# Kernel optimization log

Hardware: AMD Instinct MI355X
Metric: run time of the kernel (lower is better)

## Reference

```python
import jax, jax.numpy as jnp
import numpy as np

SEQ_LEN = 8192
D_MODEL = 1024
D_K = 128
D_V = 128


def setup_inputs() -> dict:
    key = jax.random.key(0)
    kx, kq, kk, kv = jax.random.split(key, 4)
    # xavier-uniform scale for (out, in) linear weights
    def xavier(k, out_f, in_f):
        lim = np.sqrt(6.0 / (in_f + out_f))
        return jax.random.uniform(k, (out_f, in_f), jnp.float32, -lim, lim)
    return {
        "X": jax.random.normal(kx, (SEQ_LEN, D_MODEL), jnp.float32),
        "Wq": xavier(kq, D_K, D_MODEL),
        "Wk": xavier(kk, D_K, D_MODEL),
        "Wv": xavier(kv, D_V, D_MODEL),
    }


def reference(X, Wq, Wk, Wv):
    # X: (S, d_model); W*: (d_k, d_model) torch Linear weights (y = x @ W.T)
    S = X.shape[0]
    Q = X @ Wq.T                      # (S, d_k)
    K = X @ Wk.T                      # (S, d_k)
    V = X @ Wv.T                      # (S, d_v)
    scale = jnp.sqrt(jnp.asarray(D_K, X.dtype))
    scores = (Q @ K.T) / scale        # (S, S)
    causal = jnp.tril(jnp.ones((S, S), bool))
    scores = jnp.where(causal, scores, -jnp.inf)
    weights = jax.nn.softmax(scores, axis=1)
    # dropout p=0.0 -> identity
    Z = weights @ V                   # (S, d_v)
    return Z
```

## Files before the change

### kernel.cpp

```cpp
#include <hip/hip_runtime.h>
#include <hip/hip_bf16.h>

#define S_LEN 8192
#define DM    1024
#define DK    128
#define KSTR  136
#define VSTR  72
#define SLOTD 1056

typedef __attribute__((ext_vector_type(8))) short bf16x8;
typedef __attribute__((ext_vector_type(8))) _Float16 f16x8;
typedef __attribute__((ext_vector_type(4))) float f32x4;

__device__ __forceinline__ f32x4 mfma16(bf16x8 a, bf16x8 b, f32x4 c) {
    return __builtin_amdgcn_mfma_f32_16x16x32_bf16(a, b, c, 0, 0, 0);
}

__device__ __forceinline__ ushort f2bf(float f) {
    unsigned u = __builtin_bit_cast(unsigned, f);
    u += 0x7FFFu + ((u >> 16) & 1u);
    return (ushort)(u >> 16);
}

__device__ __forceinline__ ushort f2h(float f) {
    return __builtin_bit_cast(ushort, (_Float16)f);
}

__device__ __forceinline__ uint cvt_pk_bf16(float a, float b) {
    uint r;
    asm("v_cvt_pk_bf16_f32 %0, %1, %2" : "=v"(r) : "v"(a), "v"(b));
    return r;
}

__global__ __launch_bounds__(256, 1)
void convert_kernel(const float* __restrict__ X,
                    const float* __restrict__ Wq,
                    const float* __restrict__ Wk,
                    const float* __restrict__ Wv,
                    _Float16* __restrict__ Xh,
                    _Float16* __restrict__ Wh) {
    const int NX4 = S_LEN * DM / 4;
    const int NW4 = DK * DM / 4;
    const int total4 = NX4 + 3 * NW4;
    for (int i = blockIdx.x * 256 + threadIdx.x; i < total4; i += gridDim.x * 256) {
        const float4* src;
        _Float16* dst;
        int off;
        if (i < NX4) {
            src = (const float4*)X; dst = Xh; off = i;
        } else {
            const int w = i - NX4;
            const int which = w / NW4;
            off = w - which * NW4;
            src = (const float4*)(which == 0 ? Wq : (which == 1 ? Wk : Wv));
            dst = Wh + which * (DK * DM);
        }
        const float4 v = src[off];
        union { _Float16 h[4]; uint2 u; } p;
        p.h[0] = (_Float16)v.x; p.h[1] = (_Float16)v.y;
        p.h[2] = (_Float16)v.z; p.h[3] = (_Float16)v.w;
        *(uint2*)(dst + (size_t)off * 4) = p.u;
    }
}

__global__ __launch_bounds__(256)
void proj_gemm_kernel(const _Float16* __restrict__ Xh,
                      const _Float16* __restrict__ Wh,
                      ushort* __restrict__ Qb,
                      ushort* __restrict__ Kb,
                      ushort* __restrict__ Vtb) {
    __shared__ _Float16 Ash[32 * 32];
    __shared__ _Float16 Bsh[128 * 32];

    const int tid  = threadIdx.x;
    const int lane = tid & 63;
    const int quad = lane >> 4;
    const int l15  = lane & 15;
    const int wv   = tid >> 6;
    const int wm   = wv & 1;
    const int wn   = wv >> 1;
    const int m0   = blockIdx.x * 32;
    const int nb   = blockIdx.y;
    const _Float16* Wbase = Wh + nb * (DK * DM);

    f32x4 acc[4];
#pragma unroll
    for (int ni = 0; ni < 4; ++ni) acc[ni] = (f32x4){0.f, 0.f, 0.f, 0.f};

    for (int kk = 0; kk < DM; kk += 32) {
        __syncthreads();
        for (int s = tid; s < 640; s += 256) {
            if (s < 128) {
                const int row = s >> 2, sg = s & 3;
                __builtin_amdgcn_global_load_lds(
                    (const __attribute__((address_space(1))) void*)(Xh + (size_t)(m0 + row) * DM + kk + sg * 8),
                    (__attribute__((address_space(3))) void*)(Ash + s * 8), 16, 0, 0);
            } else {
                const int t = s - 128;
                const int row = t >> 2, sg = t & 3;
                __builtin_amdgcn_global_load_lds(
                    (const __attribute__((address_space(1))) void*)(Wbase + (size_t)row * DM + kk + sg * 8),
                    (__attribute__((address_space(3))) void*)(Bsh + t * 8), 16, 0, 0);
            }
        }
        __syncthreads();

        const f16x8 af = *(const f16x8*)(Ash + (wm * 16 + l15) * 32 + quad * 8);
        f16x8 bf[4];
#pragma unroll
        for (int t = 0; t < 4; ++t)
            bf[t] = *(const f16x8*)(Bsh + (wn * 64 + t * 16 + l15) * 32 + quad * 8);
#pragma unroll
        for (int ni = 0; ni < 4; ++ni)
            acc[ni] = __builtin_amdgcn_mfma_f32_16x16x32_f16(af, bf[ni], acc[ni], 0, 0, 0);
    }

    if (nb == 2) {
#pragma unroll
        for (int ni = 0; ni < 4; ++ni) {
            const int n = wn * 64 + ni * 16 + l15;
            const int m = m0 + wm * 16 + quad * 4;
            union { ushort h[4]; uint2 u; } p;
#pragma unroll
            for (int r = 0; r < 4; ++r) p.h[r] = f2bf(acc[ni][r]);
            *(uint2*)(Vtb + (size_t)n * S_LEN + m) = p.u;
        }
    } else {
        ushort* Ob = (nb == 0) ? Qb : Kb;
        const float sc = (nb == 0) ? 0.088388347648318447f * 1.4426950408889634f : 1.0f;
#pragma unroll
        for (int ni = 0; ni < 4; ++ni) {
            const int n = wn * 64 + ni * 16 + l15;
#pragma unroll
            for (int r = 0; r < 4; ++r) {
                const int m = m0 + wm * 16 + quad * 4 + r;
                Ob[(size_t)m * DK + n] = f2bf(acc[ni][r] * sc);
            }
        }
    }
}

__global__ __launch_bounds__(256, 3)
void flash_partial_kernel(const ushort* __restrict__ Qg,
                          const ushort* __restrict__ Kg,
                          const ushort* __restrict__ Vtg,
                          float* __restrict__ Part) {
    __shared__ __align__(16) ushort Ks [64 * KSTR];
    __shared__ __align__(16) ushort Vts[128 * VSTR];

    const int b = 995 - (int)blockIdx.x;
    int qb, chunk;
    if (b < 36) {
        int q = 0;
        while (b >= (q + 1) * (q + 2) / 2) ++q;
        qb = q; chunk = b - q * (q + 1) / 2;
    } else {
        qb = 8 + ((b - 36) >> 3);
        chunk = (b - 36) & 7;
    }
    const int nkt   = qb + 1;
    const int NC    = nkt < 8 ? nkt : 8;
    const int kt_lo = chunk * nkt / NC;
    const int kt_hi = (chunk + 1) * nkt / NC;

    const int tid  = threadIdx.x;
    const int wv   = tid >> 6;
    const int lane = tid & 63;
    const int quad = lane >> 4;
    const int l15  = lane & 15;
    const int q0w  = qb * 64 + wv * 16;

    bf16x8 qf[4];
    {
        const ushort* qrow = Qg + (size_t)(q0w + l15) * DK + quad * 8;
#pragma unroll
        for (int kc = 0; kc < 4; ++kc) qf[kc] = *(const bf16x8*)(qrow + kc * 32);
    }

    float m_ = -__builtin_inff();
    float l_ = 0.f;
    f32x4 acc[8];
#pragma unroll
    for (int d = 0; d < 8; ++d) acc[d] = (f32x4){0.f, 0.f, 0.f, 0.f};

    bf16x8 stg[8];
#define LOAD_TILE(K0)                                                          \
    {                                                                          \
        const int k0_ = (K0);                                                  \
        _Pragma("unroll")                                                      \
        for (int i = 0; i < 8; ++i) {                                          \
            const int c = tid + (i << 8);                                      \
            if (c < 1024) {                                                    \
                const int row = c >> 4, ch = c & 15;                           \
                stg[i] = *(const bf16x8*)(Kg + (size_t)(k0_ + row) * DK + ch * 8); \
            } else {                                                           \
                const int cc = c - 1024;                                       \
                const int row = cc >> 3, ch = cc & 7;                          \
                stg[i] = *(const bf16x8*)(Vtg + (size_t)row * S_LEN + k0_ + ch * 8); \
            }                                                                  \
        }                                                                      \
    }

    LOAD_TILE(kt_lo * 64)

    for (int kt = kt_lo; kt < kt_hi; ++kt) {
        const int k0 = kt * 64;

        __syncthreads();
#pragma unroll
        for (int i = 0; i < 8; ++i) {
            const int c = tid + (i << 8);
            if (c < 1024) {
                const int row = c >> 4, ch = c & 15;
                *(bf16x8*)(Ks + row * KSTR + ch * 8) = stg[i];
            } else {
                const int cc = c - 1024;
                const int row = cc >> 3, ch = cc & 7;
                const int s_lo = ((ch >> 2) << 5) + ((ch & 1) << 4) + (((ch >> 1) & 1) << 2);
                union { bf16x8 v; uint2 q2[2]; } u;
                u.v = stg[i];
                ushort* vb = Vts + row * VSTR + s_lo;
                *(uint2*)vb       = u.q2[0];
                *(uint2*)(vb + 8) = u.q2[1];
            }
        }
        if (kt + 1 < kt_hi) LOAD_TILE((kt + 1) * 64)
        __syncthreads();

        f32x4 Sr[4];
        __builtin_amdgcn_s_setprio(1);
#pragma unroll
        for (int nb = 0; nb < 4; ++nb) {
            Sr[nb] = (f32x4){0.f, 0.f, 0.f, 0.f};
            const ushort* kb = Ks + (nb * 16 + l15) * KSTR + quad * 8;
#pragma unroll
            for (int kc = 0; kc < 4; ++kc)
                Sr[nb] = mfma16(*(const bf16x8*)(kb + kc * 32), qf[kc], Sr[nb]);
        }
        __builtin_amdgcn_s_setprio(0);

        if (k0 + 63 > q0w) {
            const int qg = q0w + l15;
#pragma unroll
            for (int nb = 0; nb < 4; ++nb) {
                const int kg = k0 + nb * 16 + quad * 4;
#pragma unroll
                for (int r = 0; r < 4; ++r)
                    if (kg + r > qg) Sr[nb][r] = -__builtin_inff();
            }
        }

        float pmax;
        {
            float a0 = fmaxf(fmaxf(Sr[0][0], Sr[0][1]), fmaxf(Sr[0][2], Sr[0][3]));
            float a1 = fmaxf(fmaxf(Sr[1][0], Sr[1][1]), fmaxf(Sr[1][2], Sr[1][3]));
            float a2 = fmaxf(fmaxf(Sr[2][0], Sr[2][1]), fmaxf(Sr[2][2], Sr[2][3]));
            float a3 = fmaxf(fmaxf(Sr[3][0], Sr[3][1]), fmaxf(Sr[3][2], Sr[3][3]));
            pmax = fmaxf(fmaxf(a0, a1), fmaxf(a2, a3));
            pmax = fmaxf(pmax, __shfl_xor(pmax, 16));
            pmax = fmaxf(pmax, __shfl_xor(pmax, 32));
        }
        if (__any(pmax > m_ + 8.f)) {
            const float mnew = fmaxf(m_, pmax);
            const float al = __builtin_amdgcn_exp2f(m_ - mnew);
            m_ = mnew;
            l_ *= al;
            float alr[4];
#pragma unroll
            for (int r = 0; r < 4; ++r)
                alr[r] = __shfl(al, (lane & 48) | (((lane >> 4) & 3) * 4 + r));
#pragma unroll
            for (int d = 0; d < 8; ++d)
#pragma unroll
                for (int r = 0; r < 4; ++r) acc[d][r] *= alr[r];
        }

        float p[4][4];
        float rs = 0.f;
#pragma unroll
        for (int nb = 0; nb < 4; ++nb)
#pragma unroll
            for (int r = 0; r < 4; ++r) {
                p[nb][r] = __builtin_amdgcn_exp2f(Sr[nb][r] - m_);
                rs += p[nb][r];
            }
        rs += __shfl_xor(rs, 16);
        rs += __shfl_xor(rs, 32);
        l_ += rs;

        __builtin_amdgcn_s_setprio(1);
#pragma unroll
        for (int kcp = 0; kcp < 2; ++kcp) {
            union { uint u[4]; bf16x8 v; } pf;
            pf.u[0] = cvt_pk_bf16(p[2 * kcp][0],     p[2 * kcp][1]);
            pf.u[1] = cvt_pk_bf16(p[2 * kcp][2],     p[2 * kcp][3]);
            pf.u[2] = cvt_pk_bf16(p[2 * kcp + 1][0], p[2 * kcp + 1][1]);
            pf.u[3] = cvt_pk_bf16(p[2 * kcp + 1][2], p[2 * kcp + 1][3]);
#pragma unroll
            for (int db = 0; db < 8; ++db) {
                const bf16x8 vf = *(const bf16x8*)(Vts + (db * 16 + l15) * VSTR + kcp * 32 + quad * 8);
                acc[db] = mfma16(pf.v, vf, acc[db]);
            }
        }
        __builtin_amdgcn_s_setprio(0);
    }
#undef LOAD_TILE

    const int qt16 = qb * 4 + wv;
    float* slot = Part + (size_t)(qt16 * 8 + chunk) * SLOTD;
    if (quad == 0) {
        slot[l15]      = m_;
        slot[16 + l15] = l_;
    }
    uint* slotO = (uint*)(slot + 32);
#pragma unroll
    for (int d = 0; d < 8; ++d)
#pragma unroll
        for (int r = 0; r < 4; ++r) {
            const float v  = acc[d][r];
            const float vp = __shfl_xor(v, 1);
            if ((l15 & 1) == 0) {
                const int row = quad * 4 + r;
                const uint u = (uint)f2h(v) | ((uint)f2h(vp) << 16);
                slotO[(row * 128 + d * 16 + l15) >> 1] = u;
            }
        }
}

__global__ __launch_bounds__(256)
void flash_merge_kernel(const float* __restrict__ Part, float* __restrict__ Out) {
    __shared__ float Ms[16], Ls[16];
    __shared__ float Sc[8][16];
    const int qt = blockIdx.x;
    const int q0 = qt * 16;
    const int qb = qt >> 2;
    const int P  = (qb + 1 < 8) ? (qb + 1) : 8;
    const int tid = threadIdx.x;
    const float* base = Part + (size_t)qt * 8 * SLOTD;

    if (tid < 16) {
        float M = -__builtin_inff();
        for (int p = 0; p < P; ++p) M = fmaxf(M, base[p * SLOTD + tid]);
        float L = 0.f;
        for (int p = 0; p < P; ++p)
            L += base[p * SLOTD + 16 + tid] * exp2f(base[p * SLOTD + tid] - M);
        Ms[tid] = M; Ls[tid] = L;
    }
    __syncthreads();
    if (tid < 128) {
        const int p = tid >> 4, row = tid & 15;
        Sc[p][row] = (p < P) ? exp2f(base[p * SLOTD + row] - Ms[row]) : 0.f;
    }
    __syncthreads();

#pragma unroll
    for (int j = tid; j < 1024; j += 256) {
        const int row = j >> 6, c2 = j & 63;
        float o0 = 0.f, o1 = 0.f;
        for (int p = 0; p < P; ++p) {
            const uint u = ((const uint*)(base + p * SLOTD + 32))[row * 64 + c2];
            const float sc = Sc[p][row];
            o0 += (float)__builtin_bit_cast(_Float16, (ushort)(u & 0xFFFF)) * sc;
            o1 += (float)__builtin_bit_cast(_Float16, (ushort)(u >> 16)) * sc;
        }
        const float inv = 1.0f / Ls[row];
        float2 o; o.x = o0 * inv; o.y = o1 * inv;
        *(float2*)(Out + (size_t)(q0 + row) * DK + c2 * 2) = o;
    }
}

extern "C" void kernel_launch(void* const* d_in, const int* in_sizes, int n_in,
                              void* d_out, int out_size, void* d_ws, size_t ws_size,
                              hipStream_t stream) {
    const float* X  = (const float*)d_in[0];
    const float* Wq = (const float*)d_in[1];
    const float* Wk = (const float*)d_in[2];
    const float* Wv = (const float*)d_in[3];
    ushort* ws  = (ushort*)d_ws;
    ushort* Qb  = ws;
    ushort* Kb  = ws + (size_t)S_LEN * DK;
    ushort* Vtb = ws + 2 * (size_t)S_LEN * DK;
    _Float16* Xh = (_Float16*)(ws + 3 * (size_t)S_LEN * DK);
    _Float16* Wh = Xh + (size_t)S_LEN * DM;
    float* Part = (float*)Xh;
    float* Out = (float*)d_out;

    convert_kernel<<<1024, 256, 0, stream>>>(X, Wq, Wk, Wv, Xh, Wh);
    proj_gemm_kernel<<<dim3(256, 3), 256, 0, stream>>>(Xh, Wh, Qb, Kb, Vtb);
    flash_partial_kernel<<<996, 256, 0, stream>>>(Qb, Kb, Vtb, Part);
    flash_merge_kernel<<<512, 256, 0, stream>>>(Part, Out);
}
```

Measured before the change: 158.3 us.

## Switch flash attention to 32x32 MFMA with 128-row query blocks and double-buffered LDS

Restructures the partial attention kernel so each wave handles 32 query rows using 32x32x16 bf16 MFMA instead of 16x16x32, and each block covers 128 queries. K/V tiles are double-buffered in LDS so there is one barrier per tile instead of two, and waves skip fully masked tiles. The split-K chunking is redone (up to 16 chunks per query block, 544 blocks), and the merge kernel is widened to match. This aims to raise MFMA efficiency and K/V reuse and to cut synchronization, at the cost of more registers, lower occupancy (2 blocks per CU) and larger partial buffers.

Measured after the change: 171.0 us. 8.0% more time.

```diff
diff --git a/kernel.cpp b/kernel.cpp
--- a/kernel.cpp
+++ b/kernel.cpp
@@ -6,14 +6,19 @@
 #define DK    128
 #define KSTR  136
 #define VSTR  72
-#define SLOTD 1056
+#define SLOTD 2112
+#define NCMAX 16
 
 typedef __attribute__((ext_vector_type(8))) short bf16x8;
 typedef __attribute__((ext_vector_type(8))) _Float16 f16x8;
 typedef __attribute__((ext_vector_type(4))) float f32x4;
+typedef __attribute__((ext_vector_type(16))) float f32x16;
 
 __device__ __forceinline__ f32x4 mfma16(bf16x8 a, bf16x8 b, f32x4 c) {
     return __builtin_amdgcn_mfma_f32_16x16x32_bf16(a, b, c, 0, 0, 0);
+}
+__device__ __forceinline__ f32x16 mfma32(bf16x8 a, bf16x8 b, f32x16 c) {
+    return __builtin_amdgcn_mfma_f32_32x32x16_bf16(a, b, c, 0, 0, 0);
 }
 
 __device__ __forceinline__ ushort f2bf(float f) {
@@ -140,48 +145,49 @@
     }
 }
 
-__global__ __launch_bounds__(256, 3)
+__global__ __launch_bounds__(256, 2)
 void flash_partial_kernel(const ushort* __restrict__ Qg,
                           const ushort* __restrict__ Kg,
                           const ushort* __restrict__ Vtg,
                           float* __restrict__ Part) {
-    __shared__ __align__(16) ushort Ks [64 * KSTR];
-    __shared__ __align__(16) ushort Vts[128 * VSTR];
-
-    const int b = 995 - (int)blockIdx.x;
-    int qb, chunk;
-    if (b < 36) {
-        int q = 0;
-        while (b >= (q + 1) * (q + 2) / 2) ++q;
-        qb = q; chunk = b - q * (q + 1) / 2;
-    } else {
-        qb = 8 + ((b - 36) >> 3);
-        chunk = (b - 36) & 7;
-    }
-    const int nkt   = qb + 1;
-    const int NC    = nkt < 8 ? nkt : 8;
+    __shared__ __align__(16) ushort Ks [2][64 * KSTR];
+    __shared__ __align__(16) ushort Vts[2][128 * VSTR];
+
+    int rem = 543 - (int)blockIdx.x;
+    int qb = 0;
+    for (;;) {
+        const int nc = (2 * qb + 9) >> 3;
+        if (rem < nc) break;
+        rem -= nc; ++qb;
+    }
+    const int NC    = (2 * qb + 9) >> 3;
+    const int chunk = rem;
+    const int nkt   = 2 * qb + 2;
     const int kt_lo = chunk * nkt / NC;
     const int kt_hi = (chunk + 1) * nkt / NC;
 
     const int tid  = threadIdx.x;
     const int wv   = tid >> 6;
     const int lane = tid & 63;
-    const int quad = lane >> 4;
-    const int l15  = lane & 15;
-    const int q0w  = qb * 64 + wv * 16;
-
-    bf16x8 qf[4];
+    const int l31  = lane & 31;
+    const int hi   = lane >> 5;
+    const int q0w  = qb * 128 + wv * 32;
+    const int qrow = q0w + l31;
+
+    bf16x8 qf[8];
     {
-        const ushort* qrow = Qg + (size_t)(q0w + l15) * DK + quad * 8;
-#pragma unroll
-        for (int kc = 0; kc < 4; ++kc) qf[kc] = *(const bf16x8*)(qrow + kc * 32);
+        const ushort* qp = Qg + (size_t)qrow * DK + hi * 8;
+#pragma unroll
+        for (int i = 0; i < 8; ++i) qf[i] = *(const bf16x8*)(qp + i * 16);
     }
 
     float m_ = -__builtin_inff();
     float l_ = 0.f;
-    f32x4 acc[8];
-#pragma unroll
-    for (int d = 0; d < 8; ++d) acc[d] = (f32x4){0.f, 0.f, 0.f, 0.f};
+    f32x16 acc[4];
+#pragma unroll
+    for (int dt = 0; dt < 4; ++dt)
+#pragma unroll
+        for (int j = 0; j < 16; ++j) acc[dt][j] = 0.f;
 
     bf16x8 stg[8];
 #define LOAD_TILE(K0)                                                          \
@@ -200,165 +206,174 @@
             }                                                                  \
         }                                                                      \
     }
+#define WRITE_BUF(B)                                                           \
+    {                                                                          \
+        ushort* Kb_ = Ks[B]; ushort* Vb_ = Vts[B];                             \
+        _Pragma("unroll")                                                      \
+        for (int i = 0; i < 8; ++i) {                                          \
+            const int c = tid + (i << 8);                                      \
+            if (c < 1024) {                                                    \
+                const int row = c >> 4, ch = c & 15;                           \
+                *(bf16x8*)(Kb_ + row * KSTR + ch * 8) = stg[i];                \
+            } else {                                                           \
+                const int cc = c - 1024;                                       \
+                const int row = cc >> 3, ch = cc & 7;                          \
+                const int s_lo = ((ch & 1) << 2) + (((ch >> 1) & 1) << 4) + ((ch >> 2) << 5); \
+                union { bf16x8 v; uint2 q2[2]; } u;                            \
+                u.v = stg[i];                                                  \
+                ushort* vb = Vb_ + row * VSTR + s_lo;                          \
+                *(uint2*)vb       = u.q2[0];                                   \
+                *(uint2*)(vb + 8) = u.q2[1];                                   \
+            }                                                                  \
+        }                                                                      \
+    }
 
     LOAD_TILE(kt_lo * 64)
+    WRITE_BUF(0)
+    if (kt_lo + 1 < kt_hi) LOAD_TILE((kt_lo + 1) * 64)
+    __syncthreads();
 
     for (int kt = kt_lo; kt < kt_hi; ++kt) {
         const int k0 = kt * 64;
-
+        const int cb = (kt - kt_lo) & 1;
+        const ushort* ks = Ks[cb];
+        const ushort* vs = Vts[cb];
+        const bool prc = (k0 <= q0w);
+
+        f32x16 Sr0, Sr1;
+        if (prc) {
+            __builtin_amdgcn_s_setprio(1);
+#pragma unroll
+            for (int j = 0; j < 16; ++j) { Sr0[j] = 0.f; Sr1[j] = 0.f; }
+            const ushort* ka0 = ks + l31 * KSTR + hi * 8;
+            const ushort* ka1 = ka0 + 32 * KSTR;
+#pragma unroll
+            for (int i = 0; i < 8; ++i)
+                Sr0 = mfma32(*(const bf16x8*)(ka0 + i * 16), qf[i], Sr0);
+#pragma unroll
+            for (int i = 0; i < 8; ++i)
+                Sr1 = mfma32(*(const bf16x8*)(ka1 + i * 16), qf[i], Sr1);
+            __builtin_amdgcn_s_setprio(0);
+        }
+
+        if (kt + 1 < kt_hi) {
+            WRITE_BUF(cb ^ 1)
+            if (kt + 2 < kt_hi) LOAD_TILE((kt + 2) * 64)
+        }
+
+        if (prc) {
+            if (k0 + 63 > q0w) {
+#pragma unroll
+                for (int r = 0; r < 16; ++r) {
+                    const int krow = (r & 3) + 8 * (r >> 2) + 4 * hi;
+                    if (k0 + krow > qrow)      Sr0[r] = -__builtin_inff();
+                    if (k0 + 32 + krow > qrow) Sr1[r] = -__builtin_inff();
+                }
+            }
+
+            float pmax = Sr0[0];
+#pragma unroll
+            for (int r = 1; r < 16; ++r) pmax = fmaxf(pmax, Sr0[r]);
+#pragma unroll
+            for (int r = 0; r < 16; ++r) pmax = fmaxf(pmax, Sr1[r]);
+            pmax = fmaxf(pmax, __shfl_xor(pmax, 32));
+            if (__any(pmax > m_ + 8.f)) {
+                const float mnew = fmaxf(m_, pmax);
+                const float al = __builtin_amdgcn_exp2f(m_ - mnew);
+                m_ = mnew;
+                l_ *= al;
+#pragma unroll
+                for (int dt = 0; dt < 4; ++dt)
+#pragma unroll
+                    for (int j = 0; j < 16; ++j) acc[dt][j] *= al;
+            }
+            float rs = 0.f;
+            uint pfa[16];
+            {
+                float p0[16], p1[16];
+#pragma unroll
+                for (int r = 0; r < 16; ++r) { p0[r] = __builtin_amdgcn_exp2f(Sr0[r] - m_); rs += p0[r]; }
+#pragma unroll
+                for (int r = 0; r < 16; ++r) { p1[r] = __builtin_amdgcn_exp2f(Sr1[r] - m_); rs += p1[r]; }
+#pragma unroll
+                for (int j = 0; j < 4; ++j) {
+                    pfa[j]      = cvt_pk_bf16(p0[2 * j],     p0[2 * j + 1]);
+                    pfa[4 + j]  = cvt_pk_bf16(p0[8 + 2 * j], p0[8 + 2 * j + 1]);
+                    pfa[8 + j]  = cvt_pk_bf16(p1[2 * j],     p1[2 * j + 1]);
+                    pfa[12 + j] = cvt_pk_bf16(p1[8 + 2 * j], p1[8 + 2 * j + 1]);
+                }
+            }
+            rs += __shfl_xor(rs, 32);
+            l_ += rs;
+
+            __builtin_amdgcn_s_setprio(1);
+#pragma unroll
+            for (int kc = 0; kc < 4; ++kc) {
+                union { uint u[4]; bf16x8 v; } pu;
+#pragma unroll
+                for (int j = 0; j < 4; ++j) pu.u[j] = pfa[4 * kc + j];
+                const ushort* va = vs + l31 * VSTR + kc * 16 + hi * 8;
+#pragma unroll
+                for (int dt = 0; dt < 4; ++dt)
+                    acc[dt] = mfma32(*(const bf16x8*)(va + dt * 32 * VSTR), pu.v, acc[dt]);
+            }
+            __builtin_amdgcn_s_setprio(0);
+        }
         __syncthreads();
-#pragma unroll
-        for (int i = 0; i < 8; ++i) {
-            const int c = tid + (i << 8);
-            if (c < 1024) {
-                const int row = c >> 4, ch = c & 15;
-                *(bf16x8*)(Ks + row * KSTR + ch * 8) = stg[i];
-            } else {
-                const int cc = c - 1024;
-                const int row = cc >> 3, ch = cc & 7;
-                const int s_lo = ((ch >> 2) << 5) + ((ch & 1) << 4) + (((ch >> 1) & 1) << 2);
-                union { bf16x8 v; uint2 q2[2]; } u;
-                u.v = stg[i];
-                ushort* vb = Vts + row * VSTR + s_lo;
-                *(uint2*)vb       = u.q2[0];
-                *(uint2*)(vb + 8) = u.q2[1];
-            }
-        }
-        if (kt + 1 < kt_hi) LOAD_TILE((kt + 1) * 64)
-        __syncthreads();
-
-        f32x4 Sr[4];
-        __builtin_amdgcn_s_setprio(1);
-#pragma unroll
-        for (int nb = 0; nb < 4; ++nb) {
-            Sr[nb] = (f32x4){0.f, 0.f, 0.f, 0.f};
-            const ushort* kb = Ks + (nb * 16 + l15) * KSTR + quad * 8;
-#pragma unroll
-            for (int kc = 0; kc < 4; ++kc)
-                Sr[nb] = mfma16(*(const bf16x8*)(kb + kc * 32), qf[kc], Sr[nb]);
-        }
-        __builtin_amdgcn_s_setprio(0);
-
-        if (k0 + 63 > q0w) {
-            const int qg = q0w + l15;
-#pragma unroll
-            for (int nb = 0; nb < 4; ++nb) {
-                const int kg = k0 + nb * 16 + quad * 4;
-#pragma unroll
-                for (int r = 0; r < 4; ++r)
-                    if (kg + r > qg) Sr[nb][r] = -__builtin_inff();
-            }
-        }
-
-        float pmax;
-        {
-            float a0 = fmaxf(fmaxf(Sr[0][0], Sr[0][1]), fmaxf(Sr[0][2], Sr[0][3]));
-            float a1 = fmaxf(fmaxf(Sr[1][0], Sr[1][1]), fmaxf(Sr[1][2], Sr[1][3]));
-            float a2 = fmaxf(fmaxf(Sr[2][0], Sr[2][1]), fmaxf(Sr[2][2], Sr[2][3]));
-            float a3 = fmaxf(fmaxf(Sr[3][0], Sr[3][1]), fmaxf(Sr[3][2], Sr[3][3]));
-            pmax = fmaxf(fmaxf(a0, a1), fmaxf(a2, a3));
-            pmax = fmaxf(pmax, __shfl_xor(pmax, 16));
-            pmax = fmaxf(pmax, __shfl_xor(pmax, 32));
-        }
-        if (__any(pmax > m_ + 8.f)) {
-            const float mnew = fmaxf(m_, pmax);
-            const float al = __builtin_amdgcn_exp2f(m_ - mnew);
-            m_ = mnew;
-            l_ *= al;
-            float alr[4];
-#pragma unroll
-            for (int r = 0; r < 4; ++r)
-                alr[r] = __shfl(al, (lane & 48) | (((lane >> 4) & 3) * 4 + r));
-#pragma unroll
-            for (int d = 0; d < 8; ++d)
-#pragma unroll
-                for (int r = 0; r < 4; ++r) acc[d][r] *= alr[r];
-        }
-
-        float p[4][4];
-        float rs = 0.f;
-#pragma unroll
-        for (int nb = 0; nb < 4; ++nb)
-#pragma unroll
-            for (int r = 0; r < 4; ++r) {
-                p[nb][r] = __builtin_amdgcn_exp2f(Sr[nb][r] - m_);
-                rs += p[nb][r];
-            }
-        rs += __shfl_xor(rs, 16);
-        rs += __shfl_xor(rs, 32);
-        l_ += rs;
-
-        __builtin_amdgcn_s_setprio(1);
-#pragma unroll
-        for (int kcp = 0; kcp < 2; ++kcp) {
-            union { uint u[4]; bf16x8 v; } pf;
-            pf.u[0] = cvt_pk_bf16(p[2 * kcp][0],     p[2 * kcp][1]);
-            pf.u[1] = cvt_pk_bf16(p[2 * kcp][2],     p[2 * kcp][3]);
-            pf.u[2] = cvt_pk_bf16(p[2 * kcp + 1][0], p[2 * kcp + 1][1]);
-            pf.u[3] = cvt_pk_bf16(p[2 * kcp + 1][2], p[2 * kcp + 1][3]);
-#pragma unroll
-            for (int db = 0; db < 8; ++db) {
-                const bf16x8 vf = *(const bf16x8*)(Vts + (db * 16 + l15) * VSTR + kcp * 32 + quad * 8);
-                acc[db] = mfma16(pf.v, vf, acc[db]);
-            }
-        }
-        __builtin_amdgcn_s_setprio(0);
     }
 #undef LOAD_TILE
-
-    const int qt16 = qb * 4 + wv;
-    float* slot = Part + (size_t)(qt16 * 8 + chunk) * SLOTD;
-    if (quad == 0) {
-        slot[l15]      = m_;
-        slot[16 + l15] = l_;
-    }
-    uint* slotO = (uint*)(slot + 32);
-#pragma unroll
-    for (int d = 0; d < 8; ++d)
-#pragma unroll
-        for (int r = 0; r < 4; ++r) {
-            const float v  = acc[d][r];
-            const float vp = __shfl_xor(v, 1);
-            if ((l15 & 1) == 0) {
-                const int row = quad * 4 + r;
-                const uint u = (uint)f2h(v) | ((uint)f2h(vp) << 16);
-                slotO[(row * 128 + d * 16 + l15) >> 1] = u;
-            }
+#undef WRITE_BUF
+
+    const int qt32 = qb * 4 + wv;
+    float* slot = Part + (size_t)(qt32 * NCMAX + chunk) * SLOTD;
+    if (hi == 0) {
+        slot[l31]      = m_;
+        slot[32 + l31] = l_;
+    }
+    uint* slotO = (uint*)(slot + 64);
+#pragma unroll
+    for (int dt = 0; dt < 4; ++dt)
+#pragma unroll
+        for (int s = 0; s < 4; ++s) {
+            uint2 w;
+            w.x = (uint)f2h(acc[dt][4 * s])     | ((uint)f2h(acc[dt][4 * s + 1]) << 16);
+            w.y = (uint)f2h(acc[dt][4 * s + 2]) | ((uint)f2h(acc[dt][4 * s + 3]) << 16);
+            *(uint2*)(slotO + l31 * 64 + dt * 16 + s * 4 + hi * 2) = w;
         }
 }
 
 __global__ __launch_bounds__(256)
 void flash_merge_kernel(const float* __restrict__ Part, float* __restrict__ Out) {
-    __shared__ float Ms[16], Ls[16];
-    __shared__ float Sc[8][16];
+    __shared__ float Ms[32], Ls[32];
+    __shared__ float Sc[16][32];
     const int qt = blockIdx.x;
-    const int q0 = qt * 16;
     const int qb = qt >> 2;
-    const int P  = (qb + 1 < 8) ? (qb + 1) : 8;
+    const int P  = (2 * qb + 9) >> 3;
+    const int q0 = qt * 32;
     const int tid = threadIdx.x;
-    const float* base = Part + (size_t)qt * 8 * SLOTD;
-
-    if (tid < 16) {
+    const float* base = Part + (size_t)qt * NCMAX * SLOTD;
+
+    if (tid < 32) {
         float M = -__builtin_inff();
         for (int p = 0; p < P; ++p) M = fmaxf(M, base[p * SLOTD + tid]);
         float L = 0.f;
         for (int p = 0; p < P; ++p)
-            L += base[p * SLOTD + 16 + tid] * exp2f(base[p * SLOTD + tid] - M);
+            L += base[p * SLOTD + 32 + tid] * exp2f(base[p * SLOTD + tid] - M);
         Ms[tid] = M; Ls[tid] = L;
     }
     __syncthreads();
-    if (tid < 128) {
-        const int p = tid >> 4, row = tid & 15;
+    for (int j = tid; j < 512; j += 256) {
+        const int p = j >> 5, row = j & 31;
         Sc[p][row] = (p < P) ? exp2f(base[p * SLOTD + row] - Ms[row]) : 0.f;
     }
     __syncthreads();
 
 #pragma unroll
-    for (int j = tid; j < 1024; j += 256) {
+    for (int j = tid; j < 2048; j += 256) {
         const int row = j >> 6, c2 = j & 63;
         float o0 = 0.f, o1 = 0.f;
         for (int p = 0; p < P; ++p) {
-            const uint u = ((const uint*)(base + p * SLOTD + 32))[row * 64 + c2];
+            const uint u = ((const uint*)(base + p * SLOTD + 64))[row * 64 + c2];
             const float sc = Sc[p][row];
             o0 += (float)__builtin_bit_cast(_Float16, (ushort)(u & 0xFFFF)) * sc;
             o1 += (float)__builtin_bit_cast(_Float16, (ushort)(u >> 16)) * sc;
@@ -387,6 +402,6 @@
 
     convert_kernel<<<1024, 256, 0, stream>>>(X, Wq, Wk, Wv, Xh, Wh);
     proj_gemm_kernel<<<dim3(256, 3), 256, 0, stream>>>(Xh, Wh, Qb, Kb, Vtb);
-    flash_partial_kernel<<<996, 256, 0, stream>>>(Qb, Kb, Vtb, Part);
-    flash_merge_kernel<<<512, 256, 0, stream>>>(Part, Out);
-}
+    flash_partial_kernel<<<544, 256, 0, stream>>>(Qb, Kb, Vtb, Part);
+    flash_merge_kernel<<<256, 256, 0, stream>>>(Part, Out);
+}
```

## Fuse X fp32-to-fp16 conversion into projection GEMM A-tile loads

Applied to the files above, without the earlier changes.

Removes the separate pass that converted the full X matrix to fp16, so only the weights are still converted in a small kernel. The projection GEMM now reads fp32 X directly into registers, converts each tile to fp16 as it stores it to shared memory, and prefetches the next tile across iterations. This drops a full write and reread of the 16 MB fp16 X copy. In exchange, each of the three blockIdx.y projection blocks reads and converts X separately, so fp32 X is read three times instead of once. The partial-results buffer is moved to sit after the weights in the workspace.

Result: faster. 148.8 us (-6.0%).

```diff
diff --git a/kernel.cpp b/kernel.cpp
--- a/kernel.cpp
+++ b/kernel.cpp
@@ -15,6 +15,9 @@
 __device__ __forceinline__ f32x4 mfma16(bf16x8 a, bf16x8 b, f32x4 c) {
     return __builtin_amdgcn_mfma_f32_16x16x32_bf16(a, b, c, 0, 0, 0);
 }
+__device__ __forceinline__ f32x4 mfma16f(f16x8 a, f16x8 b, f32x4 c) {
+    return __builtin_amdgcn_mfma_f32_16x16x32_f16(a, b, c, 0, 0, 0);
+}
 
 __device__ __forceinline__ ushort f2bf(float f) {
     unsigned u = __builtin_bit_cast(unsigned, f);
@@ -33,38 +36,23 @@
 }
 
 __global__ __launch_bounds__(256, 1)
-void convert_kernel(const float* __restrict__ X,
-                    const float* __restrict__ Wq,
-                    const float* __restrict__ Wk,
-                    const float* __restrict__ Wv,
-                    _Float16* __restrict__ Xh,
-                    _Float16* __restrict__ Wh) {
-    const int NX4 = S_LEN * DM / 4;
+void convert_w_kernel(const float* __restrict__ Wq,
+                      const float* __restrict__ Wk,
+                      const float* __restrict__ Wv,
+                      _Float16* __restrict__ Wh) {
     const int NW4 = DK * DM / 4;
-    const int total4 = NX4 + 3 * NW4;
-    for (int i = blockIdx.x * 256 + threadIdx.x; i < total4; i += gridDim.x * 256) {
-        const float4* src;
-        _Float16* dst;
-        int off;
-        if (i < NX4) {
-            src = (const float4*)X; dst = Xh; off = i;
-        } else {
-            const int w = i - NX4;
-            const int which = w / NW4;
-            off = w - which * NW4;
-            src = (const float4*)(which == 0 ? Wq : (which == 1 ? Wk : Wv));
-            dst = Wh + which * (DK * DM);
-        }
-        const float4 v = src[off];
-        union { _Float16 h[4]; uint2 u; } p;
-        p.h[0] = (_Float16)v.x; p.h[1] = (_Float16)v.y;
-        p.h[2] = (_Float16)v.z; p.h[3] = (_Float16)v.w;
-        *(uint2*)(dst + (size_t)off * 4) = p.u;
-    }
+    const int i = blockIdx.x * 256 + threadIdx.x;
+    const int which = i / NW4;
+    const int off = i - which * NW4;
+    const float4 v = ((const float4*)(which == 0 ? Wq : (which == 1 ? Wk : Wv)))[off];
+    union { _Float16 h[4]; uint2 u; } p;
+    p.h[0] = (_Float16)v.x; p.h[1] = (_Float16)v.y;
+    p.h[2] = (_Float16)v.z; p.h[3] = (_Float16)v.w;
+    *(uint2*)(Wh + (size_t)which * (DK * DM) + (size_t)off * 4) = p.u;
 }
 
 __global__ __launch_bounds__(256)
-void proj_gemm_kernel(const _Float16* __restrict__ Xh,
+void proj_gemm_kernel(const float* __restrict__ X,
                       const _Float16* __restrict__ Wh,
                       ushort* __restrict__ Qb,
                       ushort* __restrict__ Kb,
@@ -82,27 +70,30 @@
     const int m0   = blockIdx.x * 32;
     const int nb   = blockIdx.y;
     const _Float16* Wbase = Wh + nb * (DK * DM);
+    const int arow = tid >> 3, ac4 = tid & 7;
 
     f32x4 acc[4];
 #pragma unroll
     for (int ni = 0; ni < 4; ++ni) acc[ni] = (f32x4){0.f, 0.f, 0.f, 0.f};
+
+    float4 ra = *(const float4*)(X + (size_t)(m0 + arow) * DM + ac4 * 4);
 
     for (int kk = 0; kk < DM; kk += 32) {
         __syncthreads();
-        for (int s = tid; s < 640; s += 256) {
-            if (s < 128) {
-                const int row = s >> 2, sg = s & 3;
-                __builtin_amdgcn_global_load_lds(
-                    (const __attribute__((address_space(1))) void*)(Xh + (size_t)(m0 + row) * DM + kk + sg * 8),
-                    (__attribute__((address_space(3))) void*)(Ash + s * 8), 16, 0, 0);
-            } else {
-                const int t = s - 128;
-                const int row = t >> 2, sg = t & 3;
-                __builtin_amdgcn_global_load_lds(
-                    (const __attribute__((address_space(1))) void*)(Wbase + (size_t)row * DM + kk + sg * 8),
-                    (__attribute__((address_space(3))) void*)(Bsh + t * 8), 16, 0, 0);
-            }
-        }
+        for (int s = tid; s < 512; s += 256) {
+            const int row = s >> 2, sg = s & 3;
+            __builtin_amdgcn_global_load_lds(
+                (const __attribute__((address_space(1))) void*)(Wbase + (size_t)row * DM + kk + sg * 8),
+                (__attribute__((address_space(3))) void*)(Bsh + s * 8), 16, 0, 0);
+        }
+        {
+            union { _Float16 h[4]; uint2 u; } pa;
+            pa.h[0] = (_Float16)ra.x; pa.h[1] = (_Float16)ra.y;
+            pa.h[2] = (_Float16)ra.z; pa.h[3] = (_Float16)ra.w;
+            *(uint2*)(Ash + arow * 32 + ac4 * 4) = pa.u;
+        }
+        if (kk + 32 < DM)
+            ra = *(const float4*)(X + (size_t)(m0 + arow) * DM + kk + 32 + ac4 * 4);
         __syncthreads();
 
         const f16x8 af = *(const f16x8*)(Ash + (wm * 16 + l15) * 32 + quad * 8);
@@ -112,7 +103,7 @@
             bf[t] = *(const f16x8*)(Bsh + (wn * 64 + t * 16 + l15) * 32 + quad * 8);
 #pragma unroll
         for (int ni = 0; ni < 4; ++ni)
-            acc[ni] = __builtin_amdgcn_mfma_f32_16x16x32_f16(af, bf[ni], acc[ni], 0, 0, 0);
+            acc[ni] = mfma16f(af, bf[ni], acc[ni]);
     }
 
     if (nb == 2) {
@@ -380,13 +371,12 @@
     ushort* Qb  = ws;
     ushort* Kb  = ws + (size_t)S_LEN * DK;
     ushort* Vtb = ws + 2 * (size_t)S_LEN * DK;
-    _Float16* Xh = (_Float16*)(ws + 3 * (size_t)S_LEN * DK);
-    _Float16* Wh = Xh + (size_t)S_LEN * DM;
-    float* Part = (float*)Xh;
+    _Float16* Wh = (_Float16*)(ws + 3 * (size_t)S_LEN * DK);
+    float* Part = (float*)(Wh + (size_t)3 * DK * DM);
     float* Out = (float*)d_out;
 
-    convert_kernel<<<1024, 256, 0, stream>>>(X, Wq, Wk, Wv, Xh, Wh);
-    proj_gemm_kernel<<<dim3(256, 3), 256, 0, stream>>>(Xh, Wh, Qb, Kb, Vtb);
+    convert_w_kernel<<<384, 256, 0, stream>>>(Wq, Wk, Wv, Wh);
+    proj_gemm_kernel<<<dim3(256, 3), 256, 0, stream>>>(X, Wh, Qb, Kb, Vtb);
     flash_partial_kernel<<<996, 256, 0, stream>>>(Qb, Kb, Vtb, Part);
     flash_merge_kernel<<<512, 256, 0, stream>>>(Part, Out);
 }
```
